# Kernel tuning notes

Measured on AMD Instinct MI355X. Metric: run time of the kernel, lower is better.

The kernel has to match this reference:

```python
import jax, jax.numpy as jnp
import numpy as np

S = 2048      # seq len (q and kv)
D_MODEL = 2048
H = 16        # num heads
HD = D_MODEL // H  # head dim = 128


def softmax1(x):
    # off-by-one softmax: denominator has extra exp(-m) term (the '1' = e^0 shifted by max)
    m = jnp.maximum(jax.lax.stop_gradient(x.max(-1, keepdims=True)), 0)
    un = jnp.exp(x - m)
    return un / (jnp.exp(-m) + jnp.sum(un, axis=-1, keepdims=True))


def setup_inputs() -> dict:
    key = jax.random.key(0)
    ks = jax.random.split(key, 8)
    std = 1.0 / np.sqrt(D_MODEL)
    return {
        "query": jax.random.normal(ks[0], (S, D_MODEL), jnp.float32),
        "key_": jax.random.normal(ks[1], (S, D_MODEL), jnp.float32),
        "value": jax.random.normal(ks[2], (S, D_MODEL), jnp.float32),
        "Wq": jax.random.uniform(ks[3], (D_MODEL, D_MODEL), jnp.float32, -std, std),
        "Wk": jax.random.uniform(ks[4], (D_MODEL, D_MODEL), jnp.float32, -std, std),
        "Wv": jax.random.uniform(ks[5], (D_MODEL, D_MODEL), jnp.float32, -std, std),
        "Wo": jax.random.uniform(ks[6], (D_MODEL, D_MODEL), jnp.float32, -std, std),
        "scalars": jnp.ones((H,), jnp.float32),
    }


def reference(query, key_, value, Wq, Wk, Wv, Wo, scalars):
    # equinox Linear: y = W @ x, weight shape (out, in), no bias
    qh = (query @ Wq.T).reshape(S, H, HD)   # [S, H, HD]
    kh = (key_ @ Wk.T).reshape(S, H, HD)
    vh = (value @ Wv.T).reshape(S, H, HD)
    scale = 1.0 / jnp.sqrt(jnp.asarray(HD, qh.dtype))
    logits = jnp.einsum("qhd,khd->hqk", qh * scale, kh)  # [H, S, S]
    w = softmax1(logits)
    attn = jnp.einsum("hqk,khd->qhd", w, vh)             # [S, H, HD]
    attn = attn * scalars[None, :, None]
    return attn.reshape(S, H * HD) @ Wo.T                # [S, D_MODEL]
```

## Files before the change

### kernel.cpp

```cpp
#include <hip/hip_runtime.h>
#include <hip/hip_bf16.h>


#define S_LEN 2048
#define DMODEL 2048
#define NHEAD 16
#define HEADD 128

typedef __bf16 bf16x8 __attribute__((ext_vector_type(8)));
typedef __bf16 bf16x4 __attribute__((ext_vector_type(4)));
typedef float f32x4 __attribute__((ext_vector_type(4)));

__device__ inline void async_copy16(const __bf16* g, __bf16* l) {
    __builtin_amdgcn_global_load_lds(
        (const __attribute__((address_space(1))) unsigned int*)g,
        (__attribute__((address_space(3))) unsigned int*)l, 16, 0, 0);
}

struct CArgs {
    const float* s[8];
    __hip_bfloat16* h[8];
    __hip_bfloat16* l[8];
    float sc[8];
};

__global__ __launch_bounds__(256) void convN(CArgs a) {
    const int y = blockIdx.y;
    const float* s = a.s[y];
    __hip_bfloat16* ph = a.h[y];
    __hip_bfloat16* pl = a.l[y];
    const float sc = a.sc[y];
    size_t i4 = (size_t)blockIdx.x * 256 + threadIdx.x;
    float4 v = *(const float4*)&s[i4 * 4];
    float x0 = v.x * sc, x1 = v.y * sc, x2 = v.z * sc, x3 = v.w * sc;
    bf16x4 hv, lv;
    __bf16 a0 = (__bf16)x0, a1 = (__bf16)x1, a2 = (__bf16)x2, a3 = (__bf16)x3;
    hv[0] = a0; hv[1] = a1; hv[2] = a2; hv[3] = a3;
    lv[0] = (__bf16)(x0 - (float)a0); lv[1] = (__bf16)(x1 - (float)a1);
    lv[2] = (__bf16)(x2 - (float)a2); lv[3] = (__bf16)(x3 - (float)a3);
    *(bf16x4*)&ph[i4 * 4] = hv;
    *(bf16x4*)&pl[i4 * 4] = lv;
}

struct GArgs {
    const __bf16 *Ah, *Al, *Bh, *Bl;
    float* Cf;
    __bf16 *Ch, *Cl;
    int om;
};

__global__ __launch_bounds__(256, 2) void gemm_nt3(GArgs g0, GArgs g1, GArgs g2) {
    constexpr int K = DMODEL, N = DMODEL;
    const GArgs g = blockIdx.z == 0 ? g0 : (blockIdx.z == 1 ? g1 : g2);
    __shared__ __bf16 sAh[2][128 * 32], sAl[2][128 * 32];
    __shared__ __bf16 sBh[2][128 * 32], sBl[2][128 * 32];

    const int tid = threadIdx.x;
    const int lane = tid & 63;
    const int wave = tid >> 6;
    const int wr = wave >> 1;
    const int wc = wave & 1;
    const int qr = lane & 15;
    const int quad = lane >> 4;

    const int flat = blockIdx.y * gridDim.x + blockIdx.x;
    const int swz = (flat & 7) * 32 + (flat >> 3);
    const size_t row0 = (size_t)(swz >> 4) * 128;
    const size_t col0 = (size_t)(swz & 15) * 128;

    const int srow = tid >> 2;
    const int k8 = (((tid & 3) ^ ((tid >> 2) & 3)) * 8);
    const __bf16* gAh = g.Ah + (row0 + srow) * K + k8;
    const __bf16* gAl = g.Al + (row0 + srow) * K + k8;
    const __bf16* gBh = g.Bh + (col0 + srow) * K + k8;
    const __bf16* gBl = g.Bl + (col0 + srow) * K + k8;

    f32x4 acc[4][4] = {};

    auto stage = [&](int b, int k0) {
#pragma unroll
        for (int c = 0; c < 2; ++c) {
            async_copy16(gAh + k0 + (size_t)c * 64 * K, &sAh[b][c * 2048 + tid * 8]);
            async_copy16(gAl + k0 + (size_t)c * 64 * K, &sAl[b][c * 2048 + tid * 8]);
            async_copy16(gBh + k0 + (size_t)c * 64 * K, &sBh[b][c * 2048 + tid * 8]);
            async_copy16(gBl + k0 + (size_t)c * 64 * K, &sBl[b][c * 2048 + tid * 8]);
        }
    };

    stage(0, 0);
    __syncthreads();

    const int aslot = (quad ^ (qr & 3)) * 8;
    int cur = 0;
    for (int k0 = 0; k0 < K; k0 += 32) {
        if (k0 + 32 < K) stage(cur ^ 1, k0 + 32);

        bf16x8 a_h[4], a_l[4], b_h[4], b_l[4];
#pragma unroll
        for (int i = 0; i < 4; ++i) {
            a_h[i] = *(const bf16x8*)&sAh[cur][(wr * 64 + i * 16 + qr) * 32 + aslot];
            a_l[i] = *(const bf16x8*)&sAl[cur][(wr * 64 + i * 16 + qr) * 32 + aslot];
        }
#pragma unroll
        for (int j = 0; j < 4; ++j) {
            b_h[j] = *(const bf16x8*)&sBh[cur][(wc * 64 + j * 16 + qr) * 32 + aslot];
            b_l[j] = *(const bf16x8*)&sBl[cur][(wc * 64 + j * 16 + qr) * 32 + aslot];
        }
#pragma unroll
        for (int i = 0; i < 4; ++i)
#pragma unroll
            for (int j = 0; j < 4; ++j) {
                acc[i][j] = __builtin_amdgcn_mfma_f32_16x16x32_bf16(a_h[i], b_h[j], acc[i][j], 0, 0, 0);
                acc[i][j] = __builtin_amdgcn_mfma_f32_16x16x32_bf16(a_h[i], b_l[j], acc[i][j], 0, 0, 0);
                acc[i][j] = __builtin_amdgcn_mfma_f32_16x16x32_bf16(a_l[i], b_h[j], acc[i][j], 0, 0, 0);
            }
        __syncthreads();
        cur ^= 1;
    }

#pragma unroll
    for (int i = 0; i < 4; ++i)
#pragma unroll
        for (int j = 0; j < 4; ++j)
#pragma unroll
            for (int r = 0; r < 4; ++r) {
                size_t idx = (row0 + wr * 64 + i * 16 + quad * 4 + r) * N +
                             col0 + wc * 64 + j * 16 + qr;
                float x = acc[i][j][r];
                if (g.om == 0) {
                    g.Cf[idx] = x;
                } else if (g.om == 1) {
                    g.Ch[idx] = (__bf16)x;
                } else {
                    __bf16 hv = (__bf16)x;
                    g.Ch[idx] = hv;
                    g.Cl[idx] = (__bf16)(x - (float)hv);
                }
            }
}

__global__ __launch_bounds__(512) void attn_mfma(const __bf16* __restrict__ qhi_g,
                                                 const __bf16* __restrict__ qlo_g,
                                                 const __bf16* __restrict__ khi_g,
                                                 const __bf16* __restrict__ klo_g,
                                                 const __bf16* __restrict__ vhT,
                                                 const float* __restrict__ scalars,
                                                 __bf16* __restrict__ ohi_g,
                                                 __bf16* __restrict__ olo_g) {
    const int flatb = blockIdx.y * gridDim.x + blockIdx.x;
    const int ib = flatb >> 3;
    const int h = (flatb & 7) * 2 + (ib >> 4);
    const int q0 = (ib & 15) * 128;

    __shared__ __align__(16) __bf16 Khi[2][64][136];
    __shared__ __align__(16) __bf16 Klo[2][64][136];
    __shared__ __align__(16) __bf16 VT[2][128][72];
    __shared__ __align__(16) __bf16 Ps[128][72];

    const int tid = threadIdx.x;
    const int lane = tid & 63;
    const int wave = tid >> 6;
    const int qr = lane & 15;
    const int quad = lane >> 4;

    const int kp0 = tid >> 4;
    const int kc8 = (tid & 15) * 8;
    const int dm0 = tid >> 3;
    const int vc8 = (tid & 7) * 8;
    const __bf16* gK_hi = khi_g + (size_t)kp0 * DMODEL + h * HEADD + kc8;
    const __bf16* gK_lo = klo_g + (size_t)kp0 * DMODEL + h * HEADD + kc8;
    const __bf16* gVT = vhT + (size_t)(h * HEADD + dm0) * S_LEN + vc8;

    bf16x8 qfh[4], qfl[4];
    {
        const __bf16* qrh = qhi_g + (size_t)(q0 + wave * 16 + qr) * DMODEL + h * HEADD;
        const __bf16* qrl = qlo_g + (size_t)(q0 + wave * 16 + qr) * DMODEL + h * HEADD;
#pragma unroll
        for (int kc = 0; kc < 4; ++kc) {
            qfh[kc] = *(const bf16x8*)&qrh[kc * 32 + quad * 8];
            qfl[kc] = *(const bf16x8*)&qrl[kc * 32 + quad * 8];
        }
    }

    bf16x8 rKh[2], rKl[2], rV[2];
    auto load_regs = [&](int k0) {
#pragma unroll
        for (int i = 0; i < 2; ++i) {
            size_t go = (size_t)(k0 + i * 32) * DMODEL;
            rKh[i] = *(const bf16x8*)&gK_hi[go];
            rKl[i] = *(const bf16x8*)&gK_lo[go];
            rV[i] = *(const bf16x8*)&gVT[(size_t)(i * 64) * S_LEN + k0];
        }
    };
    auto write_lds = [&](int b) {
#pragma unroll
        for (int i = 0; i < 2; ++i) {
            *(bf16x8*)&Khi[b][kp0 + i * 32][kc8] = rKh[i];
            *(bf16x8*)&Klo[b][kp0 + i * 32][kc8] = rKl[i];
            *(bf16x8*)&VT[b][dm0 + i * 64][vc8] = rV[i];
        }
    };

    f32x4 oacc[8] = {};
    float m_r[4], l_r[4];
#pragma unroll
    for (int r = 0; r < 4; ++r) { m_r[r] = 0.f; l_r[r] = 1.f; }

    load_regs(0);
    write_lds(0);
    int cur = 0;
    for (int k0 = 0; k0 < S_LEN; k0 += 64) {
        __syncthreads();
        if (k0 + 64 < S_LEN) load_regs(k0 + 64);

        f32x4 S[4] = {};
#pragma unroll
        for (int jt = 0; jt < 4; ++jt) {
#pragma unroll
            for (int kc = 0; kc < 4; ++kc) {
                bf16x8 kh8 = *(const bf16x8*)&Khi[cur][jt * 16 + qr][kc * 32 + quad * 8];
                bf16x8 kl8 = *(const bf16x8*)&Klo[cur][jt * 16 + qr][kc * 32 + quad * 8];
                S[jt] = __builtin_amdgcn_mfma_f32_16x16x32_bf16(qfh[kc], kh8, S[jt], 0, 0, 0);
                S[jt] = __builtin_amdgcn_mfma_f32_16x16x32_bf16(qfh[kc], kl8, S[jt], 0, 0, 0);
                S[jt] = __builtin_amdgcn_mfma_f32_16x16x32_bf16(qfl[kc], kh8, S[jt], 0, 0, 0);
            }
        }

#pragma unroll
        for (int r = 0; r < 4; ++r) {
            float mx = fmaxf(fmaxf(S[0][r], S[1][r]), fmaxf(S[2][r], S[3][r]));
#pragma unroll
            for (int m = 1; m < 16; m <<= 1) mx = fmaxf(mx, __shfl_xor(mx, m, 64));
            float m_new = fmaxf(m_r[r], mx);
            float alpha = __expf(m_r[r] - m_new);
            float sum = 0.f;
            int prow = wave * 16 + quad * 4 + r;
#pragma unroll
            for (int jt = 0; jt < 4; ++jt) {
                float e = __expf(S[jt][r] - m_new);
                sum += e;
                Ps[prow][jt * 16 + qr] = (__bf16)e;
            }
#pragma unroll
            for (int m = 1; m < 16; m <<= 1) sum += __shfl_xor(sum, m, 64);
            l_r[r] = l_r[r] * alpha + sum;
            m_r[r] = m_new;
#pragma unroll
            for (int nt = 0; nt < 8; ++nt) oacc[nt][r] *= alpha;
        }

#pragma unroll
        for (int kc = 0; kc < 2; ++kc) {
            bf16x8 pf = *(const bf16x8*)&Ps[wave * 16 + qr][kc * 32 + quad * 8];
#pragma unroll
            for (int nt = 0; nt < 8; ++nt) {
                bf16x8 vf = *(const bf16x8*)&VT[cur][nt * 16 + qr][kc * 32 + quad * 8];
                oacc[nt] = __builtin_amdgcn_mfma_f32_16x16x32_bf16(pf, vf, oacc[nt], 0, 0, 0);
            }
        }

        if (k0 + 64 < S_LEN) write_lds(cur ^ 1);
        cur ^= 1;
    }

    const float sh = scalars[h];
#pragma unroll
    for (int r = 0; r < 4; ++r) {
        float wm = sh / l_r[r];
        size_t rowoff = (size_t)(q0 + wave * 16 + quad * 4 + r) * DMODEL + h * HEADD;
#pragma unroll
        for (int nt = 0; nt < 8; ++nt) {
            float x = oacc[nt][r] * wm;
            __bf16 hv = (__bf16)x;
            ohi_g[rowoff + nt * 16 + qr] = hv;
            olo_g[rowoff + nt * 16 + qr] = (__bf16)(x - (float)hv);
        }
    }
}

extern "C" void kernel_launch(void* const* d_in, const int* in_sizes, int n_in,
                              void* d_out, int out_size, void* d_ws, size_t ws_size,
                              hipStream_t stream) {
    const float* query   = (const float*)d_in[0];
    const float* key_    = (const float*)d_in[1];
    const float* value   = (const float*)d_in[2];
    const float* Wq      = (const float*)d_in[3];
    const float* Wk      = (const float*)d_in[4];
    const float* Wv      = (const float*)d_in[5];
    const float* Wo      = (const float*)d_in[6];
    const float* scalars = (const float*)d_in[7];
    float* out = (float*)d_out;

    const size_t PL = (size_t)S_LEN * DMODEL;
    __bf16* p[19];
    for (int i = 0; i < 19; ++i) p[i] = (__bf16*)d_ws + i * PL;

    const float scale = 0.08838834764831844f;
    dim3 gg(DMODEL / 128, S_LEN / 128, 1), gb(256);
    dim3 gg2(DMODEL / 128, S_LEN / 128, 2);
    dim3 gg3(DMODEL / 128, S_LEN / 128, 3);
    const int cgx = 2048 * 2048 / 4 / 256;

#define BH(x) (__hip_bfloat16*)(x)
    if (ws_size >= 19 * PL * sizeof(__bf16)) {
        {
            CArgs ca;
            ca.s[0] = query;  ca.h[0] = BH(p[0]);  ca.l[0] = BH(p[1]);  ca.sc[0] = 1.0f;
            ca.s[1] = Wq;     ca.h[1] = BH(p[2]);  ca.l[1] = BH(p[3]);  ca.sc[1] = scale;
            ca.s[2] = key_;   ca.h[2] = BH(p[4]);  ca.l[2] = BH(p[5]);  ca.sc[2] = 1.0f;
            ca.s[3] = Wk;     ca.h[3] = BH(p[6]);  ca.l[3] = BH(p[7]);  ca.sc[3] = 1.0f;
            ca.s[4] = Wv;     ca.h[4] = BH(p[12]); ca.l[4] = BH(p[13]); ca.sc[4] = 1.0f;
            ca.s[5] = value;  ca.h[5] = BH(p[14]); ca.l[5] = BH(p[15]); ca.sc[5] = 1.0f;
            ca.s[6] = Wo;     ca.h[6] = BH(p[16]); ca.l[6] = BH(p[17]); ca.sc[6] = 1.0f;
            ca.s[7] = Wo;     ca.h[7] = BH(p[16]); ca.l[7] = BH(p[17]); ca.sc[7] = 1.0f;
            convN<<<dim3(cgx, 7), 256, 0, stream>>>(ca);
        }
        {
            GArgs gq = {p[0], p[1], p[2], p[3], nullptr, p[8], p[9], 2};
            GArgs gk = {p[4], p[5], p[6], p[7], nullptr, p[10], p[11], 2};
            GArgs gv = {p[12], p[13], p[14], p[15], nullptr, p[18], nullptr, 1};
            gemm_nt3<<<gg3, gb, 0, stream>>>(gq, gk, gv);
        }
        attn_mfma<<<dim3(S_LEN / 128, NHEAD), 512, 0, stream>>>(
            p[8], p[9], p[10], p[11], p[18], scalars, p[8], p[9]);
        {
            GArgs go = {p[8], p[9], p[16], p[17], out, nullptr, nullptr, 0};
            gemm_nt3<<<gg, gb, 0, stream>>>(go, go, go);
        }
    } else {
        {
            CArgs ca;
            ca.s[0] = query; ca.h[0] = BH(p[0]); ca.l[0] = BH(p[1]); ca.sc[0] = 1.0f;
            ca.s[1] = Wq;    ca.h[1] = BH(p[2]); ca.l[1] = BH(p[3]); ca.sc[1] = scale;
            ca.s[2] = key_;  ca.h[2] = BH(p[4]); ca.l[2] = BH(p[5]); ca.sc[2] = 1.0f;
            ca.s[3] = Wk;    ca.h[3] = BH(p[6]); ca.l[3] = BH(p[7]); ca.sc[3] = 1.0f;
            convN<<<dim3(cgx, 4), 256, 0, stream>>>(ca);
        }
        {
            GArgs gq = {p[0], p[1], p[2], p[3], nullptr, p[8], p[9], 2};
            GArgs gk = {p[4], p[5], p[6], p[7], nullptr, p[10], p[11], 2};
            gemm_nt3<<<gg2, gb, 0, stream>>>(gq, gk, gk);
        }
        {
            CArgs cc;
            cc.s[0] = Wv;    cc.h[0] = BH(p[0]); cc.l[0] = BH(p[1]); cc.sc[0] = 1.0f;
            cc.s[1] = value; cc.h[1] = BH(p[2]); cc.l[1] = BH(p[3]); cc.sc[1] = 1.0f;
            cc.s[2] = Wo;    cc.h[2] = BH(p[6]); cc.l[2] = BH(p[7]); cc.sc[2] = 1.0f;
            convN<<<dim3(cgx, 3), 256, 0, stream>>>(cc);
        }
        {
            GArgs gv = {p[0], p[1], p[2], p[3], nullptr, p[4], nullptr, 1};
            gemm_nt3<<<gg, gb, 0, stream>>>(gv, gv, gv);
        }
        attn_mfma<<<dim3(S_LEN / 128, NHEAD), 512, 0, stream>>>(
            p[8], p[9], p[10], p[11], p[4], scalars, p[8], p[9]);
        {
            GArgs go = {p[8], p[9], p[6], p[7], out, nullptr, nullptr, 0};
            gemm_nt3<<<gg, gb, 0, stream>>>(go, go, go);
        }
    }
#undef BH
}
```

Baseline: 516.0 us.

## Split-K the output projection GEMM into two halves plus a reduction kernel

The output projection GEMM is split along K into two halves, run as two z-slices of the batched GEMM kernel, each writing an fp32 partial into reused workspace. A separate elementwise kernel then sums the partials into the output. This doubles the block count to fill the GPU better and improve latency hiding. The cost is extra fp32 traffic and one more launch.

Result: faster. 505.7 us (-2.0%).

```diff
diff --git a/kernel.cpp b/kernel.cpp
--- a/kernel.cpp
+++ b/kernel.cpp
@@ -42,11 +42,22 @@
     *(bf16x4*)&pl[i4 * 4] = lv;
 }
 
+__global__ __launch_bounds__(256) void addf4(float* __restrict__ o,
+                                             const float* __restrict__ a,
+                                             const float* __restrict__ b) {
+    size_t i4 = (size_t)blockIdx.x * 256 + threadIdx.x;
+    float4 va = *(const float4*)&a[i4 * 4];
+    float4 vb = *(const float4*)&b[i4 * 4];
+    float4 vo = {va.x + vb.x, va.y + vb.y, va.z + vb.z, va.w + vb.w};
+    *(float4*)&o[i4 * 4] = vo;
+}
+
 struct GArgs {
     const __bf16 *Ah, *Al, *Bh, *Bl;
     float* Cf;
     __bf16 *Ch, *Cl;
     int om;
+    int kn;
 };
 
 __global__ __launch_bounds__(256, 2) void gemm_nt3(GArgs g0, GArgs g1, GArgs g2) {
@@ -92,8 +103,8 @@
 
     const int aslot = (quad ^ (qr & 3)) * 8;
     int cur = 0;
-    for (int k0 = 0; k0 < K; k0 += 32) {
-        if (k0 + 32 < K) stage(cur ^ 1, k0 + 32);
+    for (int k0 = 0; k0 < g.kn; k0 += 32) {
+        if (k0 + 32 < g.kn) stage(cur ^ 1, k0 + 32);
 
         bf16x8 a_h[4], a_l[4], b_h[4], b_l[4];
 #pragma unroll
@@ -316,16 +327,21 @@
             convN<<<dim3(cgx, 7), 256, 0, stream>>>(ca);
         }
         {
-            GArgs gq = {p[0], p[1], p[2], p[3], nullptr, p[8], p[9], 2};
-            GArgs gk = {p[4], p[5], p[6], p[7], nullptr, p[10], p[11], 2};
-            GArgs gv = {p[12], p[13], p[14], p[15], nullptr, p[18], nullptr, 1};
+            GArgs gq = {p[0], p[1], p[2], p[3], nullptr, p[8], p[9], 2, DMODEL};
+            GArgs gk = {p[4], p[5], p[6], p[7], nullptr, p[10], p[11], 2, DMODEL};
+            GArgs gv = {p[12], p[13], p[14], p[15], nullptr, p[18], nullptr, 1, DMODEL};
             gemm_nt3<<<gg3, gb, 0, stream>>>(gq, gk, gv);
         }
         attn_mfma<<<dim3(S_LEN / 128, NHEAD), 512, 0, stream>>>(
             p[8], p[9], p[10], p[11], p[18], scalars, p[8], p[9]);
         {
-            GArgs go = {p[8], p[9], p[16], p[17], out, nullptr, nullptr, 0};
-            gemm_nt3<<<gg, gb, 0, stream>>>(go, go, go);
+            float* part0 = (float*)p[0];
+            float* part1 = (float*)p[2];
+            GArgs go0 = {p[8], p[9], p[16], p[17], part0, nullptr, nullptr, 0, 1024};
+            GArgs go1 = {p[8] + 1024, p[9] + 1024, p[16] + 1024, p[17] + 1024,
+                         part1, nullptr, nullptr, 0, 1024};
+            gemm_nt3<<<gg2, gb, 0, stream>>>(go0, go1, go1);
+            addf4<<<dim3(2048 * 2048 / 4 / 256), 256, 0, stream>>>(out, part0, part1);
         }
     } else {
         {
@@ -337,8 +353,8 @@
             convN<<<dim3(cgx, 4), 256, 0, stream>>>(ca);
         }
         {
-            GArgs gq = {p[0], p[1], p[2], p[3], nullptr, p[8], p[9], 2};
-            GArgs gk = {p[4], p[5], p[6], p[7], nullptr, p[10], p[11], 2};
+            GArgs gq = {p[0], p[1], p[2], p[3], nullptr, p[8], p[9], 2, DMODEL};
+            GArgs gk = {p[4], p[5], p[6], p[7], nullptr, p[10], p[11], 2, DMODEL};
             gemm_nt3<<<gg2, gb, 0, stream>>>(gq, gk, gk);
         }
         {
@@ -349,14 +365,19 @@
             convN<<<dim3(cgx, 3), 256, 0, stream>>>(cc);
         }
         {
-            GArgs gv = {p[0], p[1], p[2], p[3], nullptr, p[4], nullptr, 1};
+            GArgs gv = {p[0], p[1], p[2], p[3], nullptr, p[4], nullptr, 1, DMODEL};
             gemm_nt3<<<gg, gb, 0, stream>>>(gv, gv, gv);
         }
         attn_mfma<<<dim3(S_LEN / 128, NHEAD), 512, 0, stream>>>(
             p[8], p[9], p[10], p[11], p[4], scalars, p[8], p[9]);
         {
-            GArgs go = {p[8], p[9], p[6], p[7], out, nullptr, nullptr, 0};
-            gemm_nt3<<<gg, gb, 0, stream>>>(go, go, go);
+            float* part0 = (float*)p[0];
+            float* part1 = (float*)p[2];
+            GArgs go0 = {p[8], p[9], p[6], p[7], part0, nullptr, nullptr, 0, 1024};
+            GArgs go1 = {p[8] + 1024, p[9] + 1024, p[6] + 1024, p[7] + 1024,
+                         part1, nullptr, nullptr, 0, 1024};
+            gemm_nt3<<<gg2, gb, 0, stream>>>(go0, go1, go1);
+            addf4<<<dim3(2048 * 2048 / 4 / 256), 256, 0, stream>>>(out, part0, part1);
         }
     }
 #undef BH
```
